# Kernel tuning notes

Hardware: AMD Instinct MI355X
Metric: run time of the kernel (lower is better)

The kernel has to match this reference:

```python
import jax, jax.numpy as jnp
import numpy as np

B, S, K, V, H = 32, 2048, 512, 512, 256


def setup_inputs() -> dict:
    key = jax.random.key(0)
    ks = jax.random.split(key, 6)
    r = 0.1  # init_range
    return {
        "q": jax.random.normal(ks[0], (B, K), jnp.float32),
        "k": jax.random.normal(ks[1], (S, B, K), jnp.float32),
        "v": jax.random.normal(ks[2], (S, B, V), jnp.float32),
        "Wk": jax.random.uniform(ks[3], (H, K), jnp.float32, -r, r),
        "bk": jnp.zeros((H,), jnp.float32),
        "Wq": jax.random.uniform(ks[4], (H, K), jnp.float32, -r, r),
        "bq": jnp.zeros((H,), jnp.float32),
        "Wo": jax.random.uniform(ks[5], (1, H), jnp.float32, -r, r),
        "bo": jnp.zeros((1,), jnp.float32),
    }


def reference(q, k, v, Wk, bk, Wq, bq, Wo, bo):
    # k, v: [S, B, *] -> batch-first [B, S, *]
    kb = jnp.transpose(k, (1, 0, 2))  # [B, S, K]
    vb = jnp.transpose(v, (1, 0, 2))  # [B, S, V]
    h_k = jnp.einsum('bsk,hk->bsh', kb, Wk) + bk        # key2hid
    h_q = q @ Wq.T + bq                                  # [B, H]
    h = jnp.tanh(h_k + h_q[:, None, :])                  # [B, S, H]
    logit = jnp.einsum('bsh,h->bs', h, Wo[0]) + bo[0]    # hid2output, squeeze
    logit = logit - jnp.max(logit, axis=1, keepdims=True)
    p = jax.nn.softmax(logit, axis=1)                    # [B, S]
    out = jnp.sum(vb * p[:, :, None], axis=1, keepdims=True)  # [B, 1, V]
    out = jnp.transpose(out, (1, 0, 2))                  # [1, B, V]
    return out, p
```

## Files before the change

kernel.cpp:

```cpp
#include <hip/hip_runtime.h>
#include <stdint.h>

#define Bb 32
#define Ss 2048
#define Kk 512
#define Vv 512
#define Hh 256

#define OUTP (Bb * Vv)

#define WS_HQ 0
#define WS_WKB 32768
#define WS_LOGIT 294912

typedef float floatx4 __attribute__((ext_vector_type(4)));
typedef __bf16 bf16x8 __attribute__((ext_vector_type(8)));

__device__ __forceinline__ uint32_t bfround(float f) {
  uint32_t u = __float_as_uint(f);
  return (u + 0x7fffu + ((u >> 16) & 1u)) >> 16;
}
__device__ __forceinline__ uint32_t packbf(float lo, float hi) {
  return bfround(lo) | (bfround(hi) << 16);
}

__device__ __forceinline__ void gload_lds16(const uint16_t* g, uint16_t* l) {
  __builtin_amdgcn_global_load_lds((const __attribute__((address_space(1))) void*)g,
                                   (__attribute__((address_space(3))) void*)l, 16, 0, 0);
}

__global__ void prep(const float* __restrict__ q, const float* __restrict__ Wq,
                     const float* __restrict__ bq, const float* __restrict__ bk,
                     const float* __restrict__ Wk, uint16_t* __restrict__ wkb,
                     float* __restrict__ hq) {
  __shared__ float red[256];
  const int bx = blockIdx.x;
  const int t = threadIdx.x;
  if (bx < 128) {
    const int i = (bx * 256 + t) * 4;
    float4 w = *(const float4*)(Wk + i);
    const int h = i >> 9;
    const int k = i & 511;
    const int stage = k >> 5;
    const int grp = (k & 31) >> 3;
    const int j = k & 7;
    uint2 pk;
    pk.x = packbf(w.x, w.y);
    pk.y = packbf(w.z, w.w);
    *(uint2*)(wkb + stage * 8192 + (grp * 256 + h) * 8 + j) = pk;
  } else {
    const int idx = bx - 128;
    const int b = idx >> 3;
    const int hc = idx & 7;
    const int h_in = t & 31;
    const int kp = t >> 5;
    const int h = hc * 32 + h_in;
    const float4* qp = (const float4*)(q + b * Kk + kp * 64);
    const float4* wp = (const float4*)(Wq + h * Kk + kp * 64);
    float acc = 0.f;
#pragma unroll
    for (int i = 0; i < 16; ++i) {
      float4 qa = qp[i], wa = wp[i];
      acc = fmaf(qa.x, wa.x, acc);
      acc = fmaf(qa.y, wa.y, acc);
      acc = fmaf(qa.z, wa.z, acc);
      acc = fmaf(qa.w, wa.w, acc);
    }
    red[t] = acc;
    __syncthreads();
    if (t < 32) {
      float s = 0.f;
#pragma unroll
      for (int kp2 = 0; kp2 < 8; ++kp2) s += red[kp2 * 32 + t];
      const int hh = hc * 32 + t;
      hq[b * Hh + hh] = s + bq[hh] + bk[hh];
    }
  }
}

__global__ __launch_bounds__(256, 4) void fused_gemm_tanh_logit(
    const float* __restrict__ kin, const uint16_t* __restrict__ wkb,
    const float* __restrict__ hq, const float* __restrict__ Wo,
    float* __restrict__ logits) {
  __shared__ __align__(16) uint16_t lA[2][2048];
  __shared__ __align__(16) uint16_t lB[2][8192];

  const int tid = threadIdx.x;
  const int r0 = blockIdx.x * 64;
  const int wid = tid >> 6;
  const int lane = tid & 63;
  const int l15 = lane & 15;
  const int lg = lane >> 4;

  float wov[4];
#pragma unroll
  for (int ni = 0; ni < 4; ++ni) wov[ni] = Wo[wid * 64 + ni * 16 + l15];

  floatx4 acc[4][4];
#pragma unroll
  for (int mi = 0; mi < 4; ++mi)
#pragma unroll
    for (int ni = 0; ni < 4; ++ni) acc[mi][ni] = (floatx4){0.f, 0.f, 0.f, 0.f};

  const int arow = tid >> 2;
  const int apart = tid & 3;
  const float* aptr = kin + (size_t)(r0 + arow) * Kk + apart * 8;
  uint16_t* awr = &lA[0][0] + (apart * 64 + arow) * 8;

  const uint16_t* bsrc = wkb + (wid * 4) * 512 + lane * 8;
  uint16_t* bdst = &lB[0][0] + (wid * 4) * 512;

  float4 av0, av1;

#pragma unroll
  for (int it = 0; it < 4; ++it) gload_lds16(bsrc + it * 512, bdst + it * 512);
  {
    float4 a0 = *(const float4*)(aptr);
    float4 a1 = *(const float4*)(aptr + 4);
    av0 = *(const float4*)(aptr + 32);
    av1 = *(const float4*)(aptr + 36);
    uint4 w;
    w.x = packbf(a0.x, a0.y);
    w.y = packbf(a0.z, a0.w);
    w.z = packbf(a1.x, a1.y);
    w.w = packbf(a1.z, a1.w);
    *(uint4*)awr = w;
  }
  __syncthreads();

#pragma unroll
  for (int ks = 0; ks < 16; ++ks) {
    const int cur = ks & 1, nxt = cur ^ 1;
    if (ks < 15) {
#pragma unroll
      for (int it = 0; it < 4; ++it)
        gload_lds16(bsrc + (ks + 1) * 8192 + it * 512, bdst + nxt * 8192 + it * 512);
    }
    if (ks < 15) {
      uint4 w;
      w.x = packbf(av0.x, av0.y);
      w.y = packbf(av0.z, av0.w);
      w.z = packbf(av1.x, av1.y);
      w.w = packbf(av1.z, av1.w);
      *(uint4*)(awr + nxt * 2048) = w;
    }
    if (ks < 14) {
      av0 = *(const float4*)(aptr + (ks + 2) * 32);
      av1 = *(const float4*)(aptr + (ks + 2) * 32 + 4);
    }
    {
      bf16x8 af[4], bfr[4];
#pragma unroll
      for (int mi = 0; mi < 4; ++mi)
        af[mi] = *(const bf16x8*)&lA[cur][(lg * 64 + mi * 16 + l15) * 8];
#pragma unroll
      for (int ni = 0; ni < 4; ++ni)
        bfr[ni] = *(const bf16x8*)&lB[cur][(lg * 256 + wid * 64 + ni * 16 + l15) * 8];
#pragma unroll
      for (int mi = 0; mi < 4; ++mi)
#pragma unroll
        for (int ni = 0; ni < 4; ++ni)
          acc[mi][ni] = __builtin_amdgcn_mfma_f32_16x16x32_bf16(
              af[mi], bfr[ni], acc[mi][ni], 0, 0, 0);
    }
    if (ks < 15) __syncthreads();
  }

  float* lpart = (float*)&lA[0][0];
#pragma unroll
  for (int pp = 0; pp < 2; ++pp) {
    float hqv[4][4];
#pragma unroll
    for (int r = 0; r < 4; ++r)
#pragma unroll
      for (int ni = 0; ni < 4; ++ni)
        hqv[r][ni] = hq[(pp * 16 + lg * 4 + r) * Hh + wid * 64 + ni * 16 + l15];
#pragma unroll
    for (int mm = 0; mm < 2; ++mm) {
      const int mi = pp + mm * 2;
#pragma unroll
      for (int r = 0; r < 4; ++r) {
        float sum = 0.f;
#pragma unroll
        for (int ni = 0; ni < 4; ++ni) {
          const float x = acc[mi][ni][r] + hqv[r][ni];
          const float e = __expf(2.f * x);
          const float th = 1.f - 2.f * __builtin_amdgcn_rcpf(e + 1.f);
          sum = fmaf(th, wov[ni], sum);
        }
        sum += __shfl_xor(sum, 1, 64);
        sum += __shfl_xor(sum, 2, 64);
        sum += __shfl_xor(sum, 4, 64);
        sum += __shfl_xor(sum, 8, 64);
        if (l15 == 0) lpart[wid * 64 + mi * 16 + lg * 4 + r] = sum;
      }
    }
  }
  __syncthreads();
  if (tid < 64) {
    const float lv = lpart[0 * 64 + tid] + lpart[1 * 64 + tid] +
                     lpart[2 * 64 + tid] + lpart[3 * 64 + tid];
    logits[(tid & 31) * Ss + (r0 >> 5) + (tid >> 5)] = lv;
  }
}

__global__ void softmax_zero(const float* __restrict__ logits, float* __restrict__ dout) {
  const int b = blockIdx.x;
  const int t = threadIdx.x;
  const int wid = t >> 6, lane = t & 63;
  __shared__ float red[4];
  const float4* lp = (const float4*)(logits + b * Ss);
  const float4 x0 = lp[t * 2], x1 = lp[t * 2 + 1];
  float mx = fmaxf(fmaxf(fmaxf(x0.x, x0.y), fmaxf(x0.z, x0.w)),
                   fmaxf(fmaxf(x1.x, x1.y), fmaxf(x1.z, x1.w)));
#pragma unroll
  for (int off = 1; off < 64; off <<= 1) mx = fmaxf(mx, __shfl_xor(mx, off, 64));
  if (lane == 0) red[wid] = mx;
  __syncthreads();
  mx = fmaxf(fmaxf(red[0], red[1]), fmaxf(red[2], red[3]));
  __syncthreads();
  float e[8];
  e[0] = __expf(x0.x - mx); e[1] = __expf(x0.y - mx);
  e[2] = __expf(x0.z - mx); e[3] = __expf(x0.w - mx);
  e[4] = __expf(x1.x - mx); e[5] = __expf(x1.y - mx);
  e[6] = __expf(x1.z - mx); e[7] = __expf(x1.w - mx);
  float s = ((e[0] + e[1]) + (e[2] + e[3])) + ((e[4] + e[5]) + (e[6] + e[7]));
#pragma unroll
  for (int off = 1; off < 64; off <<= 1) s += __shfl_xor(s, off, 64);
  if (lane == 0) red[wid] = s;
  __syncthreads();
  s = (red[0] + red[1]) + (red[2] + red[3]);
  const float inv = 1.f / s;
  float4 p0, p1;
  p0.x = e[0] * inv; p0.y = e[1] * inv; p0.z = e[2] * inv; p0.w = e[3] * inv;
  p1.x = e[4] * inv; p1.y = e[5] * inv; p1.z = e[6] * inv; p1.w = e[7] * inv;
  float4* pout = (float4*)(dout + OUTP + b * Ss);
  pout[t * 2] = p0;
  pout[t * 2 + 1] = p1;
  dout[b * Vv + t] = 0.f;
  dout[b * Vv + 256 + t] = 0.f;
}

__global__ __launch_bounds__(256) void weighted_vsum(const float* __restrict__ v,
                                                     float* __restrict__ dout) {
  const int sc = blockIdx.x;
  const int b = blockIdx.y;
  const int t = threadIdx.x;
  __shared__ float lp[128];
  if (t < 128) lp[t] = dout[OUTP + b * Ss + sc * 128 + t];
  __syncthreads();
  const int c4 = t & 127;
  const int sh = t >> 7;
  float4 acc = {0.f, 0.f, 0.f, 0.f};
#pragma unroll 8
  for (int i = 0; i < 64; ++i) {
    const int sl = sh + 2 * i;
    const int s = sc * 128 + sl;
    const float4 vv = *(const float4*)(v + ((size_t)s * Bb + b) * Vv + c4 * 4);
    const float pw = lp[sl];
    acc.x = fmaf(pw, vv.x, acc.x);
    acc.y = fmaf(pw, vv.y, acc.y);
    acc.z = fmaf(pw, vv.z, acc.z);
    acc.w = fmaf(pw, vv.w, acc.w);
  }
  float* o = dout + b * Vv + c4 * 4;
  atomicAdd(o + 0, acc.x);
  atomicAdd(o + 1, acc.y);
  atomicAdd(o + 2, acc.z);
  atomicAdd(o + 3, acc.w);
}

extern "C" void kernel_launch(void* const* d_in, const int* in_sizes, int n_in,
                              void* d_out, int out_size, void* d_ws, size_t ws_size,
                              hipStream_t stream) {
  const float* q  = (const float*)d_in[0];
  const float* k  = (const float*)d_in[1];
  const float* v  = (const float*)d_in[2];
  const float* Wk = (const float*)d_in[3];
  const float* bk = (const float*)d_in[4];
  const float* Wq = (const float*)d_in[5];
  const float* bq = (const float*)d_in[6];
  const float* Wo = (const float*)d_in[7];

  float* out = (float*)d_out;
  char* ws = (char*)d_ws;
  float* hq = (float*)(ws + WS_HQ);
  uint16_t* wkb = (uint16_t*)(ws + WS_WKB);
  float* logits = (float*)(ws + WS_LOGIT);

  prep<<<dim3(384), dim3(256), 0, stream>>>(q, Wq, bq, bk, Wk, wkb, hq);
  fused_gemm_tanh_logit<<<dim3((Ss * Bb) / 64), dim3(256), 0, stream>>>(k, wkb, hq, Wo, logits);
  softmax_zero<<<dim3(Bb), dim3(256), 0, stream>>>(logits, out);
  weighted_vsum<<<dim3(16, Bb), dim3(256), 0, stream>>>(v, out);
}
```

Baseline: 312.7 us.

## Fuse weighted V sum into GEMM-tanh kernel and drop softmax max pass

The GEMM kernel now covers one batch and 64 sequence positions per block. Each block exponentiates its logits directly, stores the unnormalised weights, and accumulates the weighted sum of V into the output with atomics. A small finalize kernel then normalises the probabilities and the output row by the sum. The output zeroing moves into an extra prep block. This removes a kernel launch and a separate pass that re-read the logits, and it overlaps the V stream with the GEMM work. In exchange it doubles the atomic count, reads K with a strided row pattern, and skips max subtraction. That relies on the logits staying bounded, since |tanh| ≤ 1 and Wo is small.

```diff
diff --git a/kernel.cpp b/kernel.cpp
--- a/kernel.cpp
+++ b/kernel.cpp
@@ -32,7 +32,7 @@
 __global__ void prep(const float* __restrict__ q, const float* __restrict__ Wq,
                      const float* __restrict__ bq, const float* __restrict__ bk,
                      const float* __restrict__ Wk, uint16_t* __restrict__ wkb,
-                     float* __restrict__ hq) {
+                     float* __restrict__ hq, float* __restrict__ dout) {
   __shared__ float red[256];
   const int bx = blockIdx.x;
   const int t = threadIdx.x;
@@ -48,7 +48,7 @@
     pk.x = packbf(w.x, w.y);
     pk.y = packbf(w.z, w.w);
     *(uint2*)(wkb + stage * 8192 + (grp * 256 + h) * 8 + j) = pk;
-  } else {
+  } else if (bx < 384) {
     const int idx = bx - 128;
     const int b = idx >> 3;
     const int hc = idx & 7;
@@ -75,26 +75,37 @@
       const int hh = hc * 32 + t;
       hq[b * Hh + hh] = s + bq[hh] + bk[hh];
     }
+  } else {
+    float4 z = {0.f, 0.f, 0.f, 0.f};
+    float4* o = (float4*)dout + t;
+#pragma unroll
+    for (int i = 0; i < 16; ++i) o[i * 256] = z;
   }
 }
 
 __global__ __launch_bounds__(256, 4) void fused_gemm_tanh_logit(
     const float* __restrict__ kin, const uint16_t* __restrict__ wkb,
     const float* __restrict__ hq, const float* __restrict__ Wo,
-    float* __restrict__ logits) {
+    float* __restrict__ wlog, const float* __restrict__ vin,
+    float* __restrict__ dout) {
   __shared__ __align__(16) uint16_t lA[2][2048];
   __shared__ __align__(16) uint16_t lB[2][8192];
 
   const int tid = threadIdx.x;
-  const int r0 = blockIdx.x * 64;
+  const int sc = blockIdx.x;
+  const int b = blockIdx.y;
   const int wid = tid >> 6;
   const int lane = tid & 63;
   const int l15 = lane & 15;
   const int lg = lane >> 4;
 
-  float wov[4];
-#pragma unroll
-  for (int ni = 0; ni < 4; ++ni) wov[ni] = Wo[wid * 64 + ni * 16 + l15];
+  float hqv[4], wov[4];
+#pragma unroll
+  for (int ni = 0; ni < 4; ++ni) {
+    const int n = wid * 64 + ni * 16 + l15;
+    hqv[ni] = hq[b * Hh + n];
+    wov[ni] = Wo[n];
+  }
 
   floatx4 acc[4][4];
 #pragma unroll
@@ -104,7 +115,7 @@
 
   const int arow = tid >> 2;
   const int apart = tid & 3;
-  const float* aptr = kin + (size_t)(r0 + arow) * Kk + apart * 8;
+  const float* aptr = kin + ((size_t)((sc * 64 + arow) * Bb) + b) * Kk + apart * 8;
   uint16_t* awr = &lA[0][0] + (apart * 64 + arow) * 8;
 
   const uint16_t* bsrc = wkb + (wid * 4) * 512 + lane * 8;
@@ -167,64 +178,57 @@
   }
 
   float* lpart = (float*)&lA[0][0];
-#pragma unroll
-  for (int pp = 0; pp < 2; ++pp) {
-    float hqv[4][4];
-#pragma unroll
-    for (int r = 0; r < 4; ++r)
-#pragma unroll
-      for (int ni = 0; ni < 4; ++ni)
-        hqv[r][ni] = hq[(pp * 16 + lg * 4 + r) * Hh + wid * 64 + ni * 16 + l15];
-#pragma unroll
-    for (int mm = 0; mm < 2; ++mm) {
-      const int mi = pp + mm * 2;
-#pragma unroll
-      for (int r = 0; r < 4; ++r) {
-        float sum = 0.f;
-#pragma unroll
-        for (int ni = 0; ni < 4; ++ni) {
-          const float x = acc[mi][ni][r] + hqv[r][ni];
-          const float e = __expf(2.f * x);
-          const float th = 1.f - 2.f * __builtin_amdgcn_rcpf(e + 1.f);
-          sum = fmaf(th, wov[ni], sum);
-        }
-        sum += __shfl_xor(sum, 1, 64);
-        sum += __shfl_xor(sum, 2, 64);
-        sum += __shfl_xor(sum, 4, 64);
-        sum += __shfl_xor(sum, 8, 64);
-        if (l15 == 0) lpart[wid * 64 + mi * 16 + lg * 4 + r] = sum;
+  float* sw = (float*)&lA[0][0] + 256;
+#pragma unroll
+  for (int mi = 0; mi < 4; ++mi) {
+#pragma unroll
+    for (int r = 0; r < 4; ++r) {
+      float sum = 0.f;
+#pragma unroll
+      for (int ni = 0; ni < 4; ++ni) {
+        const float x = acc[mi][ni][r] + hqv[ni];
+        const float e = __expf(2.f * x);
+        const float th = 1.f - 2.f * __builtin_amdgcn_rcpf(e + 1.f);
+        sum = fmaf(th, wov[ni], sum);
       }
+      sum += __shfl_xor(sum, 1, 64);
+      sum += __shfl_xor(sum, 2, 64);
+      sum += __shfl_xor(sum, 4, 64);
+      sum += __shfl_xor(sum, 8, 64);
+      if (l15 == 0) lpart[wid * 64 + mi * 16 + lg * 4 + r] = sum;
     }
   }
   __syncthreads();
   if (tid < 64) {
-    const float lv = lpart[0 * 64 + tid] + lpart[1 * 64 + tid] +
-                     lpart[2 * 64 + tid] + lpart[3 * 64 + tid];
-    logits[(tid & 31) * Ss + (r0 >> 5) + (tid >> 5)] = lv;
-  }
-}
-
-__global__ void softmax_zero(const float* __restrict__ logits, float* __restrict__ dout) {
+    const float lv = lpart[tid] + lpart[64 + tid] + lpart[128 + tid] + lpart[192 + tid];
+    const float w = __expf(lv);
+    wlog[b * Ss + sc * 64 + tid] = w;
+    sw[tid] = w;
+  }
+  __syncthreads();
+
+  const int c = tid * 2;
+  float ax = 0.f, ay = 0.f;
+#pragma unroll 8
+  for (int s = 0; s < 64; ++s) {
+    const float2 vv = *(const float2*)(vin + ((size_t)((sc * 64 + s) * Bb) + b) * Vv + c);
+    const float pw = sw[s];
+    ax = fmaf(pw, vv.x, ax);
+    ay = fmaf(pw, vv.y, ay);
+  }
+  float* o = dout + b * Vv + c;
+  atomicAdd(o + 0, ax);
+  atomicAdd(o + 1, ay);
+}
+
+__global__ void finalize(const float* __restrict__ wlog, float* __restrict__ dout) {
   const int b = blockIdx.x;
   const int t = threadIdx.x;
   const int wid = t >> 6, lane = t & 63;
   __shared__ float red[4];
-  const float4* lp = (const float4*)(logits + b * Ss);
-  const float4 x0 = lp[t * 2], x1 = lp[t * 2 + 1];
-  float mx = fmaxf(fmaxf(fmaxf(x0.x, x0.y), fmaxf(x0.z, x0.w)),
-                   fmaxf(fmaxf(x1.x, x1.y), fmaxf(x1.z, x1.w)));
-#pragma unroll
-  for (int off = 1; off < 64; off <<= 1) mx = fmaxf(mx, __shfl_xor(mx, off, 64));
-  if (lane == 0) red[wid] = mx;
-  __syncthreads();
-  mx = fmaxf(fmaxf(red[0], red[1]), fmaxf(red[2], red[3]));
-  __syncthreads();
-  float e[8];
-  e[0] = __expf(x0.x - mx); e[1] = __expf(x0.y - mx);
-  e[2] = __expf(x0.z - mx); e[3] = __expf(x0.w - mx);
-  e[4] = __expf(x1.x - mx); e[5] = __expf(x1.y - mx);
-  e[6] = __expf(x1.z - mx); e[7] = __expf(x1.w - mx);
-  float s = ((e[0] + e[1]) + (e[2] + e[3])) + ((e[4] + e[5]) + (e[6] + e[7]));
+  const float4* wp = (const float4*)(wlog + b * Ss);
+  const float4 x0 = wp[t * 2], x1 = wp[t * 2 + 1];
+  float s = ((x0.x + x0.y) + (x0.z + x0.w)) + ((x1.x + x1.y) + (x1.z + x1.w));
 #pragma unroll
   for (int off = 1; off < 64; off <<= 1) s += __shfl_xor(s, off, 64);
   if (lane == 0) red[wid] = s;
@@ -232,42 +236,16 @@
   s = (red[0] + red[1]) + (red[2] + red[3]);
   const float inv = 1.f / s;
   float4 p0, p1;
-  p0.x = e[0] * inv; p0.y = e[1] * inv; p0.z = e[2] * inv; p0.w = e[3] * inv;
-  p1.x = e[4] * inv; p1.y = e[5] * inv; p1.z = e[6] * inv; p1.w = e[7] * inv;
+  p0.x = x0.x * inv; p0.y = x0.y * inv; p0.z = x0.z * inv; p0.w = x0.w * inv;
+  p1.x = x1.x * inv; p1.y = x1.y * inv; p1.z = x1.z * inv; p1.w = x1.w * inv;
   float4* pout = (float4*)(dout + OUTP + b * Ss);
   pout[t * 2] = p0;
   pout[t * 2 + 1] = p1;
-  dout[b * Vv + t] = 0.f;
-  dout[b * Vv + 256 + t] = 0.f;
-}
-
-__global__ __launch_bounds__(256) void weighted_vsum(const float* __restrict__ v,
-                                                     float* __restrict__ dout) {
-  const int sc = blockIdx.x;
-  const int b = blockIdx.y;
-  const int t = threadIdx.x;
-  __shared__ float lp[128];
-  if (t < 128) lp[t] = dout[OUTP + b * Ss + sc * 128 + t];
-  __syncthreads();
-  const int c4 = t & 127;
-  const int sh = t >> 7;
-  float4 acc = {0.f, 0.f, 0.f, 0.f};
-#pragma unroll 8
-  for (int i = 0; i < 64; ++i) {
-    const int sl = sh + 2 * i;
-    const int s = sc * 128 + sl;
-    const float4 vv = *(const float4*)(v + ((size_t)s * Bb + b) * Vv + c4 * 4);
-    const float pw = lp[sl];
-    acc.x = fmaf(pw, vv.x, acc.x);
-    acc.y = fmaf(pw, vv.y, acc.y);
-    acc.z = fmaf(pw, vv.z, acc.z);
-    acc.w = fmaf(pw, vv.w, acc.w);
-  }
-  float* o = dout + b * Vv + c4 * 4;
-  atomicAdd(o + 0, acc.x);
-  atomicAdd(o + 1, acc.y);
-  atomicAdd(o + 2, acc.z);
-  atomicAdd(o + 3, acc.w);
+  float2* op = (float2*)(dout + b * Vv + t * 2);
+  float2 ov = *op;
+  ov.x *= inv;
+  ov.y *= inv;
+  *op = ov;
 }
 
 extern "C" void kernel_launch(void* const* d_in, const int* in_sizes, int n_in,
@@ -286,10 +264,9 @@
   char* ws = (char*)d_ws;
   float* hq = (float*)(ws + WS_HQ);
   uint16_t* wkb = (uint16_t*)(ws + WS_WKB);
-  float* logits = (float*)(ws + WS_LOGIT);
-
-  prep<<<dim3(384), dim3(256), 0, stream>>>(q, Wq, bq, bk, Wk, wkb, hq);
-  fused_gemm_tanh_logit<<<dim3((Ss * Bb) / 64), dim3(256), 0, stream>>>(k, wkb, hq, Wo, logits);
-  softmax_zero<<<dim3(Bb), dim3(256), 0, stream>>>(logits, out);
-  weighted_vsum<<<dim3(16, Bb), dim3(256), 0, stream>>>(v, out);
-}
+  float* wlog = (float*)(ws + WS_LOGIT);
+
+  prep<<<dim3(385), dim3(256), 0, stream>>>(q, Wq, bq, bk, Wk, wkb, hq, out);
+  fused_gemm_tanh_logit<<<dim3(Ss / 64, Bb), dim3(256), 0, stream>>>(k, wkb, hq, Wo, wlog, v, out);
+  finalize<<<dim3(Bb), dim3(256), 0, stream>>>(wlog, out);
+}
```

Measured after the change: 299.7 us. 1.04x faster.
